# Kernel optimization log

Measured on AMD Instinct MI355X. Metric: run time of the kernel, lower is better.

Reference implementation:

```python
import jax, jax.numpy as jnp
import numpy as np


def setup_inputs() -> dict:
    key = jax.random.key(0)
    ks = jax.random.split(key, 4)
    B, Tq, Tv = 8, 1024, 1024
    Dq, Dv, Do = 1024, 1024, 1024
    scale_q = 1.0 / np.sqrt(Dq)
    scale_2 = 1.0 / np.sqrt(Dq + Dv)
    return {
        "query": jax.random.normal(ks[0], (B, Tq, Dq), jnp.float32),
        "values": jax.random.normal(ks[1], (B, Tv, Dv), jnp.float32),
        "W1": jax.random.normal(ks[2], (Dv, Dq), jnp.float32) * scale_q,
        "b1": jnp.zeros((Dv,), jnp.float32),
        "W2": jax.random.normal(ks[3], (Do, Dq + Dv), jnp.float32) * scale_2,
        "b2": jnp.zeros((Do,), jnp.float32),
    }


def reference(query, values, W1, b1, W2, b2):
    # linear1: project query into values space  [B, Tq, Dv]
    q_resize = jnp.einsum("btd,vd->btv", query, W1) + b1
    # attention scores [B, Tq, Tv] and softmax over keys
    scores = jnp.einsum("bqd,bkd->bqk", q_resize, values)
    attn = jax.nn.softmax(scores, axis=-1)
    # attended values [B, Tq, Dv]
    attended = jnp.einsum("bqk,bkd->bqd", attn, values)
    # concat + linear2 + tanh
    feed = jnp.concatenate([attended, query], axis=-1)
    out = jnp.tanh(jnp.einsum("btf,of->bto", feed, W2) + b2)
    return out
```

## Files before the change

kernel.cpp:

```cpp
#include <hip/hip_runtime.h>
#include <hip/hip_bf16.h>

typedef __bf16 bf16x8 __attribute__((ext_vector_type(8)));
typedef float f32x4 __attribute__((ext_vector_type(4)));
typedef unsigned short u16;
typedef unsigned short us4 __attribute__((ext_vector_type(4)));
typedef unsigned int u32;

__device__ __forceinline__ u16 f2bf(float x) {
  union { float f; u32 u; } v; v.f = x;
  u32 r = v.u + 0x7FFFu + ((v.u >> 16) & 1u);
  return (u16)(r >> 16);
}
__device__ __forceinline__ float bf2f(u16 h) {
  union { u32 u; float f; } v; v.u = ((u32)h) << 16;
  return v.f;
}

__device__ __forceinline__ void glds16(const void* g, void* l) {
  __builtin_amdgcn_global_load_lds(
      (const __attribute__((address_space(1))) void*)g,
      (__attribute__((address_space(3))) void*)l, 16, 0, 0);
}

template<int NSEG, int EPI>
__global__ __launch_bounds__(512)
void gemm_bt(const u16* __restrict__ A, const u16* __restrict__ B,
             void* __restrict__ Cout, const float* __restrict__ bias,
             int K0, int lda, int ldb, int ldc,
             long sA, long sB, long sC, int nx, int ny)
{
  __shared__ __align__(16) u16 As[2][2][256 * 32];
  __shared__ __align__(16) u16 Bs[2][2][128 * 32];

  const int d = blockIdx.x;
  const int L = ((d & 7) << 5) | (d >> 3);
  const int nxy = nx * ny;
  const int bz = L / nxy;
  const int rr = L - bz * nxy;
  const int bx = rr / ny;
  const int by = rr - bx * ny;
  const int brow = bx * 256;
  const int bcol = by * 128;

  const int tid  = threadIdx.x;
  const int wid  = tid >> 6;
  const int lane = tid & 63;
  const int wr   = wid >> 1;
  const int wc   = wid & 1;

  const u16* Ab = A + (long)bz * sA + (long)brow * lda;
  const u16* Bb = B + (long)bz * sB + (long)bcol * ldb;

  f32x4 acc[4][4];
#pragma unroll
  for (int m = 0; m < 4; ++m)
#pragma unroll
    for (int n = 0; n < 4; ++n) acc[m][n] = (f32x4){0.f, 0.f, 0.f, 0.f};

  const int sr = lane >> 2;
  const int sc = (lane & 3) * 8;

  const int ksteps = (NSEG == 3) ? 16 : (K0 >> 6);
  const int NT = NSEG * ksteps;

  auto stage = [&](int buf, int t) {
    int seg, kt;
    if (NSEG == 3) { seg = t >> 4; kt = (t & 15) << 6; }
    else           { seg = 0;      kt = t << 6; }
    const u16* Aseg = Ab + ((NSEG == 3 && seg == 1) ? K0 : 0) + kt;
    const u16* Bseg = Bb + ((NSEG == 3 && seg == 2) ? K0 : 0) + kt;
#pragma unroll
    for (int h = 0; h < 2; ++h) {
#pragma unroll
      for (int i = 0; i < 2; ++i) {
        const int row = wid * 32 + i * 16;
        glds16(Aseg + (long)(row + sr) * lda + h * 32 + sc,
               As[buf][h] + row * 32);
      }
      {
        const int row = wid * 16;
        glds16(Bseg + (long)(row + sr) * ldb + h * 32 + sc,
               Bs[buf][h] + row * 32);
      }
    }
  };

  const int lr = lane & 15;
  const int lk = (lane >> 4) * 8;

  stage(0, 0);
  __syncthreads();

  int buf = 0;
  for (int t = 0; t < NT; ++t) {
    if (t + 1 < NT) stage(buf ^ 1, t + 1);
#pragma unroll
    for (int h = 0; h < 2; ++h) {
      bf16x8 af[4], bfr[4];
#pragma unroll
      for (int m = 0; m < 4; ++m)
        af[m] = *(const bf16x8*)(As[buf][h] + (wr * 64 + m * 16 + lr) * 32 + lk);
#pragma unroll
      for (int n = 0; n < 4; ++n)
        bfr[n] = *(const bf16x8*)(Bs[buf][h] + (wc * 64 + n * 16 + lr) * 32 + lk);
#pragma unroll
      for (int m = 0; m < 4; ++m)
#pragma unroll
        for (int n = 0; n < 4; ++n)
          acc[m][n] = __builtin_amdgcn_mfma_f32_16x16x32_bf16(af[m], bfr[n], acc[m][n], 0, 0, 0);
    }
    __syncthreads();
    buf ^= 1;
  }

  const int crow0 = brow + wr * 64;
  const int ccol0 = bcol + wc * 64;
  const int orow  = (lane >> 4) * 4;
  const int ocol  = lane & 15;

#pragma unroll
  for (int m = 0; m < 4; ++m) {
#pragma unroll
    for (int n = 0; n < 4; ++n) {
      const int col = ccol0 + n * 16 + ocol;
      float bv = 0.f;
      if (EPI == 1 || EPI == 3) bv = bias[col];
#pragma unroll
      for (int j = 0; j < 4; ++j) {
        const int row = crow0 + m * 16 + orow + j;
        float v = acc[m][n][j] + bv;
        if (EPI == 0) {
          ((float*)Cout)[(long)bz * sC + (long)row * ldc + col] = v;
        } else if (EPI == 1) {
          u16 hi = f2bf(v);
          u16 lo = f2bf(v - bf2f(hi));
          u16* Co = (u16*)Cout + (long)bz * sC + (long)row * ldc;
          Co[col] = hi;
          Co[col + 1024] = lo;
        } else if (EPI == 2) {
          ((u16*)Cout)[(long)bz * sC + (long)row * ldc + col] = f2bf(v);
        } else {
          ((float*)Cout)[(long)bz * sC + (long)row * ldc + col] = tanhf(v);
        }
      }
    }
  }
}

__global__ __launch_bounds__(256)
void split_pack(const float* __restrict__ X, u16* __restrict__ P,
                u16* __restrict__ FQ, long n4)
{
  long i = (long)blockIdx.x * 256 + threadIdx.x;
  const long stride = (long)gridDim.x * 256;
  for (; i < n4; i += stride) {
    float4 x = ((const float4*)X)[i];
    long e = i * 4;
    long row = e >> 10;
    int col = (int)(e & 1023);
    float xs[4] = {x.x, x.y, x.z, x.w};
    u16 h[4], l[4];
#pragma unroll
    for (int j = 0; j < 4; ++j) {
      h[j] = f2bf(xs[j]);
      l[j] = f2bf(xs[j] - bf2f(h[j]));
    }
    us4 hv = {h[0], h[1], h[2], h[3]};
    us4 lv = {l[0], l[1], l[2], l[3]};
    *(us4*)(P + row * 2048 + col) = hv;
    *(us4*)(P + row * 2048 + 1024 + col) = lv;
    if (FQ) *(us4*)(FQ + row * 2048 + 1024 + col) = hv;
  }
}

__global__ __launch_bounds__(256)
void conv_values(const float* __restrict__ V, u16* __restrict__ Vp,
                 u16* __restrict__ VT)
{
  __shared__ u16 tile[64][68];
  const int b  = blockIdx.z;
  const int d0 = blockIdx.x * 64;
  const int k0 = blockIdx.y * 64;
  const int t  = threadIdx.x;
  const int tr = t >> 4;
  const int tc = (t & 15) * 4;
  const float* Vb = V + (long)b * (1024L * 1024);
  u16* Vpb = Vp + (long)b * (1024L * 2048);
  u16* VTb = VT + (long)b * (1024L * 1024);

#pragma unroll
  for (int i = 0; i < 4; ++i) {
    int k = tr + i * 16;
    float4 x = *(const float4*)(Vb + (long)(k0 + k) * 1024 + d0 + tc);
    float xs[4] = {x.x, x.y, x.z, x.w};
    u16 h[4], l[4];
#pragma unroll
    for (int j = 0; j < 4; ++j) {
      h[j] = f2bf(xs[j]);
      l[j] = f2bf(xs[j] - bf2f(h[j]));
      tile[k][tc + j] = h[j];
    }
    us4 hv = {h[0], h[1], h[2], h[3]};
    us4 lv = {l[0], l[1], l[2], l[3]};
    *(us4*)(Vpb + (long)(k0 + k) * 2048 + d0 + tc) = hv;
    *(us4*)(Vpb + (long)(k0 + k) * 2048 + 1024 + d0 + tc) = lv;
  }
  __syncthreads();
#pragma unroll
  for (int i = 0; i < 4; ++i) {
    int d = tr + i * 16;
    int k = tc;
    us4 o = {tile[k][d], tile[k + 1][d], tile[k + 2][d], tile[k + 3][d]};
    *(us4*)(VTb + (long)(d0 + d) * 1024 + k0 + k) = o;
  }
}

__global__ __launch_bounds__(256)
void conv_cast(const float* __restrict__ X, u16* __restrict__ Y, long n4)
{
  long i = (long)blockIdx.x * 256 + threadIdx.x;
  const long stride = (long)gridDim.x * 256;
  for (; i < n4; i += stride) {
    float4 x = ((const float4*)X)[i];
    us4 o = {f2bf(x.x), f2bf(x.y), f2bf(x.z), f2bf(x.w)};
    *(us4*)(Y + i * 4) = o;
  }
}

__global__ __launch_bounds__(256)
void softmax_rows(const float* __restrict__ S, u16* __restrict__ A)
{
  const long row = blockIdx.x;
  const float* src = S + row * 1024;
  const int t = threadIdx.x;
  const int lane = t & 63, wid = t >> 6;
  float4 v = ((const float4*)src)[t];
  float m = fmaxf(fmaxf(v.x, v.y), fmaxf(v.z, v.w));
#pragma unroll
  for (int off = 32; off >= 1; off >>= 1)
    m = fmaxf(m, __shfl_xor(m, off));
  __shared__ float redm[4];
  if (lane == 0) redm[wid] = m;
  __syncthreads();
  m = fmaxf(fmaxf(redm[0], redm[1]), fmaxf(redm[2], redm[3]));
  float e0 = __expf(v.x - m), e1 = __expf(v.y - m);
  float e2 = __expf(v.z - m), e3 = __expf(v.w - m);
  float s = e0 + e1 + e2 + e3;
#pragma unroll
  for (int off = 32; off >= 1; off >>= 1)
    s += __shfl_xor(s, off);
  __shared__ float reds[4];
  if (lane == 0) reds[wid] = s;
  __syncthreads();
  s = reds[0] + reds[1] + reds[2] + reds[3];
  float inv = 1.0f / s;
  us4 o = {f2bf(e0 * inv), f2bf(e1 * inv), f2bf(e2 * inv), f2bf(e3 * inv)};
  ((us4*)(A + row * 1024))[t] = o;
}

extern "C" void kernel_launch(void* const* d_in, const int* in_sizes, int n_in,
                              void* d_out, int out_size, void* d_ws, size_t ws_size,
                              hipStream_t stream)
{
  const float* query  = (const float*)d_in[0];
  const float* values = (const float*)d_in[1];
  const float* W1     = (const float*)d_in[2];
  const float* b1     = (const float*)d_in[3];
  const float* W2     = (const float*)d_in[4];
  const float* b2     = (const float*)d_in[5];
  float* out = (float*)d_out;

  char* ws = (char*)d_ws;
  const long MB = 1024L * 1024;
  u16*   W1p    = (u16*)(ws);
  u16*   W2b    = (u16*)(ws + 4 * MB);
  u16*   Aq     = (u16*)(ws + 8 * MB);
  float* scores = (float*)(ws + 8 * MB);
  u16*   qr     = (u16*)(ws + 40 * MB);
  u16*   attn   = (u16*)(ws + 40 * MB);
  u16*   Vp     = (u16*)(ws + 72 * MB);
  u16*   VT     = (u16*)(ws + 104 * MB);
  u16*   feed   = (u16*)(ws + 120 * MB);

  split_pack<<<dim3(2048), dim3(256), 0, stream>>>(query, Aq, feed, (8192L * 1024) / 4);
  split_pack<<<dim3(1024), dim3(256), 0, stream>>>(W1, W1p, (u16*)nullptr, (1024L * 1024) / 4);
  conv_values<<<dim3(16, 16, 8), dim3(256), 0, stream>>>(values, Vp, VT);
  conv_cast<<<dim3(1024), dim3(256), 0, stream>>>(W2, W2b, (1024L * 2048) / 4);

  gemm_bt<3, 1><<<dim3(256), dim3(512), 0, stream>>>(
      Aq, W1p, qr, b1, 1024, 2048, 2048, 2048, 0L, 0L, 0L, 32, 8);

  gemm_bt<3, 0><<<dim3(256), dim3(512), 0, stream>>>(
      qr, Vp, scores, (const float*)nullptr, 1024, 2048, 2048, 1024,
      1024L * 2048, 1024L * 2048, 1024L * 1024, 4, 8);

  softmax_rows<<<dim3(8192), dim3(256), 0, stream>>>(scores, attn);

  gemm_bt<1, 2><<<dim3(256), dim3(512), 0, stream>>>(
      attn, VT, feed, (const float*)nullptr, 1024, 1024, 1024, 2048,
      1024L * 1024, 1024L * 1024, 1024L * 2048, 4, 8);

  gemm_bt<1, 3><<<dim3(256), dim3(512), 0, stream>>>(
      feed, W2b, out, b2, 2048, 2048, 2048, 1024, 0L, 0L, 0L, 32, 8);
}
```

Measured before the change: 390.6 us.

## Triple-buffer GEMM with fragment-major LDS layout and intra-block split-K

The bf16 GEMM kernel now uses a three-stage LDS ring with two k-tiles in flight, using explicit vmcnt waits and fenced barriers in place of double buffering with __syncthreads. The LDS tiles are stored fragment-major, so each lane reads one contiguous 16-byte MFMA fragment, which is meant to avoid bank conflicts and address arithmetic. The eight waves split each 64-wide k-tile into two halves, each covering a larger 128x64 output per wave. The halves are then reduced through LDS before the epilogue. MFMA priority is raised with setprio and launch bounds request 2 blocks per CU. In exchange, the kernel doubles the accumulator registers (spill risk under the occupancy hint), uses about 144KB of LDS, and adds a reduction pass.

```diff
diff --git a/kernel.cpp b/kernel.cpp
--- a/kernel.cpp
+++ b/kernel.cpp
@@ -23,15 +23,20 @@
       (__attribute__((address_space(3))) void*)l, 16, 0, 0);
 }
 
+#define BARRIER_FENCED() do {                        \
+  __builtin_amdgcn_sched_barrier(0);                 \
+  __builtin_amdgcn_s_barrier();                      \
+  __builtin_amdgcn_sched_barrier(0);                 \
+} while (0)
+
 template<int NSEG, int EPI>
-__global__ __launch_bounds__(512)
+__global__ __launch_bounds__(512, 2)
 void gemm_bt(const u16* __restrict__ A, const u16* __restrict__ B,
              void* __restrict__ Cout, const float* __restrict__ bias,
              int K0, int lda, int ldb, int ldc,
              long sA, long sB, long sC, int nx, int ny)
 {
-  __shared__ __align__(16) u16 As[2][2][256 * 32];
-  __shared__ __align__(16) u16 Bs[2][2][128 * 32];
+  __shared__ __align__(1024) char lds_raw[3 * 49152];
 
   const int d = blockIdx.x;
   const int L = ((d & 7) << 5) | (d >> 3);
@@ -46,102 +51,129 @@
   const int tid  = threadIdx.x;
   const int wid  = tid >> 6;
   const int lane = tid & 63;
-  const int wr   = wid >> 1;
+  const int kh   = wid >> 2;
+  const int wr   = (wid >> 1) & 1;
   const int wc   = wid & 1;
 
   const u16* Ab = A + (long)bz * sA + (long)brow * lda;
   const u16* Bb = B + (long)bz * sB + (long)bcol * ldb;
 
-  f32x4 acc[4][4];
-#pragma unroll
-  for (int m = 0; m < 4; ++m)
+  f32x4 acc[8][4];
+#pragma unroll
+  for (int m = 0; m < 8; ++m)
 #pragma unroll
     for (int n = 0; n < 4; ++n) acc[m][n] = (f32x4){0.f, 0.f, 0.f, 0.f};
-
-  const int sr = lane >> 2;
-  const int sc = (lane & 3) * 8;
 
   const int ksteps = (NSEG == 3) ? 16 : (K0 >> 6);
   const int NT = NSEG * ksteps;
 
-  auto stage = [&](int buf, int t) {
+  const int r15 = lane & 15;
+  const int c16 = (lane >> 4) * 8;
+
+  auto stage = [&](int t, int b) {
     int seg, kt;
     if (NSEG == 3) { seg = t >> 4; kt = (t & 15) << 6; }
     else           { seg = 0;      kt = t << 6; }
     const u16* Aseg = Ab + ((NSEG == 3 && seg == 1) ? K0 : 0) + kt;
     const u16* Bseg = Bb + ((NSEG == 3 && seg == 2) ? K0 : 0) + kt;
-#pragma unroll
-    for (int h = 0; h < 2; ++h) {
-#pragma unroll
-      for (int i = 0; i < 2; ++i) {
-        const int row = wid * 32 + i * 16;
-        glds16(Aseg + (long)(row + sr) * lda + h * 32 + sc,
-               As[buf][h] + row * 32);
-      }
-      {
-        const int row = wid * 16;
-        glds16(Bseg + (long)(row + sr) * ldb + h * 32 + sc,
-               Bs[buf][h] + row * 32);
-      }
+    u16* Lb = (u16*)(lds_raw + b * 49152);
+#pragma unroll
+    for (int q = 0; q < 4; ++q) {
+      const int fa = wid * 4 + q;
+      const int mi = fa >> 1, ki = fa & 1;
+      glds16(Aseg + (long)(mi * 16 + r15) * lda + ki * 32 + c16, Lb + fa * 512);
+    }
+#pragma unroll
+    for (int q = 0; q < 2; ++q) {
+      const int fb = wid * 2 + q;
+      const int nj = fb >> 1, ki = fb & 1;
+      glds16(Bseg + (long)(nj * 16 + r15) * ldb + ki * 32 + c16,
+             Lb + 16384 + fb * 512);
     }
   };
 
-  const int lr = lane & 15;
-  const int lk = (lane >> 4) * 8;
-
   stage(0, 0);
-  __syncthreads();
-
-  int buf = 0;
+  stage(1, 1);
+  asm volatile("s_waitcnt vmcnt(6)" ::: "memory");
+  BARRIER_FENCED();
+
+  int bufc = 0;
   for (int t = 0; t < NT; ++t) {
-    if (t + 1 < NT) stage(buf ^ 1, t + 1);
-#pragma unroll
-    for (int h = 0; h < 2; ++h) {
-      bf16x8 af[4], bfr[4];
-#pragma unroll
-      for (int m = 0; m < 4; ++m)
-        af[m] = *(const bf16x8*)(As[buf][h] + (wr * 64 + m * 16 + lr) * 32 + lk);
+    const u16* Lb = (const u16*)(lds_raw + bufc * 49152);
+    const u16* Af = Lb + (wr * 16 + kh) * 512 + lane * 8;
+    const u16* Bf = Lb + 16384 + (wc * 8 + kh) * 512 + lane * 8;
+    bf16x8 a[8], b[4];
+#pragma unroll
+    for (int m = 0; m < 8; ++m) a[m] = *(const bf16x8*)(Af + m * 1024);
+#pragma unroll
+    for (int n = 0; n < 4; ++n) b[n] = *(const bf16x8*)(Bf + n * 1024);
+
+    if (t + 2 < NT) {
+      int bufs = bufc + 2; if (bufs >= 3) bufs -= 3;
+      stage(t + 2, bufs);
+    }
+
+    __builtin_amdgcn_s_setprio(1);
+#pragma unroll
+    for (int m = 0; m < 8; ++m)
 #pragma unroll
       for (int n = 0; n < 4; ++n)
-        bfr[n] = *(const bf16x8*)(Bs[buf][h] + (wc * 64 + n * 16 + lr) * 32 + lk);
-#pragma unroll
-      for (int m = 0; m < 4; ++m)
-#pragma unroll
-        for (int n = 0; n < 4; ++n)
-          acc[m][n] = __builtin_amdgcn_mfma_f32_16x16x32_bf16(af[m], bfr[n], acc[m][n], 0, 0, 0);
-    }
-    __syncthreads();
-    buf ^= 1;
-  }
-
-  const int crow0 = brow + wr * 64;
-  const int ccol0 = bcol + wc * 64;
-  const int orow  = (lane >> 4) * 4;
-  const int ocol  = lane & 15;
-
-#pragma unroll
-  for (int m = 0; m < 4; ++m) {
-#pragma unroll
-    for (int n = 0; n < 4; ++n) {
-      const int col = ccol0 + n * 16 + ocol;
-      float bv = 0.f;
-      if (EPI == 1 || EPI == 3) bv = bias[col];
-#pragma unroll
-      for (int j = 0; j < 4; ++j) {
-        const int row = crow0 + m * 16 + orow + j;
-        float v = acc[m][n][j] + bv;
-        if (EPI == 0) {
-          ((float*)Cout)[(long)bz * sC + (long)row * ldc + col] = v;
-        } else if (EPI == 1) {
-          u16 hi = f2bf(v);
-          u16 lo = f2bf(v - bf2f(hi));
-          u16* Co = (u16*)Cout + (long)bz * sC + (long)row * ldc;
-          Co[col] = hi;
-          Co[col + 1024] = lo;
-        } else if (EPI == 2) {
-          ((u16*)Cout)[(long)bz * sC + (long)row * ldc + col] = f2bf(v);
-        } else {
-          ((float*)Cout)[(long)bz * sC + (long)row * ldc + col] = tanhf(v);
+        acc[m][n] = __builtin_amdgcn_mfma_f32_16x16x32_bf16(a[m], b[n], acc[m][n], 0, 0, 0);
+    __builtin_amdgcn_s_setprio(0);
+
+    if (t + 2 < NT) { asm volatile("s_waitcnt vmcnt(6)" ::: "memory"); }
+    else            { asm volatile("s_waitcnt vmcnt(0)" ::: "memory"); }
+    BARRIER_FENCED();
+    bufc = bufc + 1; if (bufc >= 3) bufc = 0;
+  }
+
+  float* red = (float*)lds_raw;
+  const int p = wr * 2 + wc;
+  if (kh == 1) {
+#pragma unroll
+    for (int m = 0; m < 8; ++m)
+#pragma unroll
+      for (int n = 0; n < 4; ++n)
+        *(f32x4*)(red + ((p * 32 + m * 4 + n) * 64 + lane) * 4) = acc[m][n];
+  }
+  asm volatile("s_waitcnt lgkmcnt(0)" ::: "memory");
+  BARRIER_FENCED();
+
+  if (kh == 0) {
+#pragma unroll
+    for (int m = 0; m < 8; ++m)
+#pragma unroll
+      for (int n = 0; n < 4; ++n)
+        acc[m][n] += *(const f32x4*)(red + ((p * 32 + m * 4 + n) * 64 + lane) * 4);
+
+    const int crow0 = brow + wr * 128;
+    const int ccol0 = bcol + wc * 64;
+    const int orow  = (lane >> 4) * 4;
+    const int ocol  = lane & 15;
+#pragma unroll
+    for (int m = 0; m < 8; ++m) {
+#pragma unroll
+      for (int n = 0; n < 4; ++n) {
+        const int col = ccol0 + n * 16 + ocol;
+        float bv = 0.f;
+        if (EPI == 1 || EPI == 3) bv = bias[col];
+#pragma unroll
+        for (int j = 0; j < 4; ++j) {
+          const int row = crow0 + m * 16 + orow + j;
+          float v = acc[m][n][j] + bv;
+          if (EPI == 0) {
+            ((float*)Cout)[(long)bz * sC + (long)row * ldc + col] = v;
+          } else if (EPI == 1) {
+            u16 hi = f2bf(v);
+            u16 lo = f2bf(v - bf2f(hi));
+            u16* Co = (u16*)Cout + (long)bz * sC + (long)row * ldc;
+            Co[col] = hi;
+            Co[col + 1024] = lo;
+          } else if (EPI == 2) {
+            ((u16*)Cout)[(long)bz * sC + (long)row * ldc + col] = f2bf(v);
+          } else {
+            ((float*)Cout)[(long)bz * sC + (long)row * ldc + col] = tanhf(v);
+          }
         }
       }
     }
```

Measured after the change: 395.2 us. No clear change (+1.2%).
